# Kernel tuning notes

Hardware: AMD Instinct MI355X
Metric: run time of the kernel (lower is better)

Reference implementation:

```python
import jax, jax.numpy as jnp
import numpy as np

N_NODES = 50000


def graph_conv(h, src, dst, W, b, num_nodes):
    """GCN-style conv: transform node features, then sum messages over edges.
    h: [N, Din], W: [Din, Dout] -> out: [N, Dout].
    """
    m = (h @ W)[src]                                   # [E, Dout] per-edge messages
    agg = jax.ops.segment_sum(m, dst, num_segments=num_nodes)  # [N, Dout]
    return agg + b


def setup_inputs() -> dict:
    key = jax.random.key(0)
    ks = jax.random.split(key, 8)
    N, E, D = N_NODES, 800000, 128
    s = 1.0 / np.sqrt(2 * D)
    return {
        "node_feature": jax.random.normal(ks[0], (N, D), jnp.float32),
        "H_prev": jax.random.normal(ks[1], (N, D), jnp.float32),
        "edge_index": jax.random.randint(ks[2], (2, E), 0, N, jnp.int32),
        "W_main": jax.random.normal(ks[3], (D, D), jnp.float32) / np.sqrt(D),
        "b_main": jnp.zeros((D,), jnp.float32),
        "W_z": jax.random.normal(ks[4], (2 * D, D), jnp.float32) * s,
        "b_z": jnp.zeros((D,), jnp.float32),
        "W_r": jax.random.normal(ks[5], (2 * D, D), jnp.float32) * s,
        "b_r": jnp.zeros((D,), jnp.float32),
        "W_h": jax.random.normal(ks[6], (2 * D, D), jnp.float32) * s,
        "b_h": jnp.zeros((D,), jnp.float32),
    }


def reference(node_feature, H_prev, edge_index, W_main, b_main,
              W_z, b_z, W_r, b_r, W_h, b_h):
    N = node_feature.shape[0]
    src, dst = edge_index[0], edge_index[1]
    # main message-passing layer + post-layer activation (ReLU)
    X = jax.nn.relu(graph_conv(node_feature, src, dst, W_main, b_main, N))
    # GRU-gated graph convolutions
    cat_zr = jnp.concatenate([X, H_prev], axis=1)       # [N, 2D]
    Z = jax.nn.sigmoid(graph_conv(cat_zr, src, dst, W_z, b_z, N))
    R = jax.nn.sigmoid(graph_conv(cat_zr, src, dst, W_r, b_r, N))
    cat_h = jnp.concatenate([X, R * H_prev], axis=1)
    H_tilde = jnp.tanh(graph_conv(cat_h, src, dst, W_h, b_h, N))
    H_out = Z * H_prev + (1.0 - Z) * H_tilde
    return H_out
```

## Files before the change

### kernel.cpp

```cpp
#include <hip/hip_runtime.h>
#include <hip/hip_fp16.h>
#include <math.h>

typedef _Float16 f16;
typedef f16 f16x2 __attribute__((ext_vector_type(2)));
typedef f16 f16x4 __attribute__((ext_vector_type(4)));
typedef f16 f16x8 __attribute__((ext_vector_type(8)));
typedef float f32x4_t __attribute__((ext_vector_type(4)));

__device__ __forceinline__ float sigmoidf(float x) {
  return 1.0f / (1.0f + __expf(-x));
}

#define GLDS16(gp, lp)                                                     \
  __builtin_amdgcn_global_load_lds(                                        \
      (const __attribute__((address_space(1))) void*)(gp),                 \
      (__attribute__((address_space(3))) void*)(lp), 16, 0, 0)

__global__ void zero_ints(int* __restrict__ p, int n) {
  int i = blockIdx.x * blockDim.x + threadIdx.x;
  if (i < n) p[i] = 0;
}

__global__ void count_kernel(const int* __restrict__ dst, int* __restrict__ cnt, int E) {
  int base = (blockIdx.x * blockDim.x + threadIdx.x) * 4;
  if (base + 3 < E) {
    int4 d = *(const int4*)&dst[base];
    atomicAdd(&cnt[d.x], 1);
    atomicAdd(&cnt[d.y], 1);
    atomicAdd(&cnt[d.z], 1);
    atomicAdd(&cnt[d.w], 1);
  } else {
    for (int e = base; e < E; ++e) atomicAdd(&cnt[dst[e]], 1);
  }
}

__global__ __launch_bounds__(1024) void scan_local(const int* __restrict__ cnt,
                                                   int* __restrict__ off,
                                                   int* __restrict__ psum, int n) {
  __shared__ int wsum[16];
  const int tid = threadIdx.x, lane = tid & 63, wid = tid >> 6;
  int i = blockIdx.x * 1024 + tid;
  int v = (i < n) ? cnt[i] : 0;
  int x = v;
  #pragma unroll
  for (int d = 1; d < 64; d <<= 1) { int y = __shfl_up(x, d); if (lane >= d) x += y; }
  if (lane == 63) wsum[wid] = x;
  __syncthreads();
  if (wid == 0) {
    int ws = (lane < 16) ? wsum[lane] : 0;
    #pragma unroll
    for (int d = 1; d < 16; d <<= 1) { int y = __shfl_up(ws, d); if (lane >= d) ws += y; }
    if (lane < 16) wsum[lane] = ws;
  }
  __syncthreads();
  int excl = x - v + (wid ? wsum[wid - 1] : 0);
  if (i < n) off[i] = excl;
  if (tid == 1023) psum[blockIdx.x] = wsum[15];
}

__global__ __launch_bounds__(1024) void scan_carry(int* __restrict__ psum,
                                                   int* __restrict__ off,
                                                   int* __restrict__ cur, int nb, int n) {
  __shared__ int wsum[16];
  const int tid = threadIdx.x, lane = tid & 63, wid = tid >> 6;
  int v = (tid < nb) ? psum[tid] : 0;
  int x = v;
  #pragma unroll
  for (int d = 1; d < 64; d <<= 1) { int y = __shfl_up(x, d); if (lane >= d) x += y; }
  if (lane == 63) wsum[wid] = x;
  __syncthreads();
  if (wid == 0) {
    int ws = (lane < 16) ? wsum[lane] : 0;
    #pragma unroll
    for (int d = 1; d < 16; d <<= 1) { int y = __shfl_up(ws, d); if (lane >= d) ws += y; }
    if (lane < 16) wsum[lane] = ws;
  }
  __syncthreads();
  int excl = x - v + (wid ? wsum[wid - 1] : 0);
  if (tid < nb) psum[tid] = excl;
  if (tid == 1023) { off[n] = wsum[15]; cur[n] = wsum[15]; }
}

__global__ __launch_bounds__(1024) void scan_add(int* __restrict__ off, int* __restrict__ cur,
                                                 const int* __restrict__ psum, int n) {
  int i = blockIdx.x * 1024 + threadIdx.x;
  if (i < n) {
    int t = off[i] + psum[blockIdx.x];
    off[i] = t;
    cur[i] = t;
  }
}

template <typename IDX>
__global__ void fill_kernel(const int* __restrict__ src, const int* __restrict__ dst,
                            int* __restrict__ cur, IDX* __restrict__ eidx, int E) {
  int base = (blockIdx.x * blockDim.x + threadIdx.x) * 4;
  if (base + 3 < E) {
    int4 d = *(const int4*)&dst[base];
    int4 s = *(const int4*)&src[base];
    int p0 = atomicAdd(&cur[d.x], 1);
    int p1 = atomicAdd(&cur[d.y], 1);
    int p2 = atomicAdd(&cur[d.z], 1);
    int p3 = atomicAdd(&cur[d.w], 1);
    eidx[p0] = (IDX)s.x;
    eidx[p1] = (IDX)s.y;
    eidx[p2] = (IDX)s.z;
    eidx[p3] = (IDX)s.w;
  } else {
    for (int e = base; e < E; ++e) {
      int p = atomicAdd(&cur[dst[e]], 1);
      eidx[p] = (IDX)src[e];
    }
  }
}

__global__ void pack_nfh(const float* __restrict__ nf, const float* __restrict__ H,
                         f16* __restrict__ P0, int N) {
  int gid = blockIdx.x * blockDim.x + threadIdx.x;
  int w = gid >> 6;
  if (w >= N) return;
  int lane = threadIdx.x & 63;
  const float* S = (lane < 32) ? nf : H;
  int c = (lane & 31) * 4;
  float4 u = *(const float4*)&S[(size_t)w * 128 + c];
  f16x4 o = {(f16)u.x, (f16)u.y, (f16)u.z, (f16)u.w};
  *(f16x4*)&P0[(size_t)w * 256 + (lane < 32 ? 0 : 128) + c] = o;
}

__global__ void wtrans_all(const float* __restrict__ Wm, const float* __restrict__ Wz,
                           const float* __restrict__ Wr, const float* __restrict__ Wh,
                           f16* __restrict__ WtM, f16* __restrict__ WtZR,
                           f16* __restrict__ WtH) {
  __shared__ float tile[32][33];
  const float* W;
  f16* O;
  int K;
  switch (blockIdx.z) {
    case 0: W = Wm; O = WtM; K = 128; break;
    case 1: W = Wz; O = WtZR; K = 256; break;
    case 2: W = Wr; O = WtZR + 128 * 256; K = 256; break;
    default: W = Wh; O = WtH; K = 256; break;
  }
  int bk = blockIdx.x * 32, bn = blockIdx.y * 32;
  if (bk >= K) return;
  int tx = threadIdx.x, ty = threadIdx.y;
  #pragma unroll
  for (int i = 0; i < 4; ++i)
    tile[ty + 8 * i][tx] = W[(size_t)(bk + ty + 8 * i) * 128 + bn + tx];
  __syncthreads();
  #pragma unroll
  for (int i = 0; i < 4; ++i)
    O[(size_t)(bn + ty + 8 * i) * K + bk + tx] = (f16)tile[tx][ty + 8 * i];
}

template <int COLS, typename IDX>
__global__ __launch_bounds__(256) void gather(const f16* __restrict__ P,
                                              const int* __restrict__ off,
                                              const IDX* __restrict__ eidx,
                                              f16* __restrict__ O, int N) {
  int gid = blockIdx.x * blockDim.x + threadIdx.x;
  int w = __builtin_amdgcn_readfirstlane(gid >> 6);
  if (w >= N) return;
  const int lane = threadIdx.x & 63;
  const int beg = off[w], end = off[w + 1];
  const char* base = (const char*)P;
  constexpr int SH = (COLS == 256) ? 9 : 8;
  int j = beg;
  if constexpr (COLS == 256) {
    const int lb = lane * 8;
    float a0 = 0.f, a1 = 0.f, a2 = 0.f, a3 = 0.f;
    for (; j + 8 <= end; j += 8) {
      f16x4 v[8];
      #pragma unroll
      for (int u = 0; u < 8; ++u)
        v[u] = *(const f16x4*)(base + (((int)eidx[j + u]) << SH) + lb);
      #pragma unroll
      for (int u = 0; u < 8; ++u) {
        a0 += (float)v[u].x; a1 += (float)v[u].y;
        a2 += (float)v[u].z; a3 += (float)v[u].w;
      }
    }
    for (; j < end; ++j) {
      f16x4 v = *(const f16x4*)(base + (((int)eidx[j]) << SH) + lb);
      a0 += (float)v.x; a1 += (float)v.y; a2 += (float)v.z; a3 += (float)v.w;
    }
    f16x4 o = {(f16)a0, (f16)a1, (f16)a2, (f16)a3};
    *(f16x4*)&O[(size_t)w * 256 + lane * 4] = o;
  } else {
    const int lb = lane * 4;
    float a0 = 0.f, a1 = 0.f;
    for (; j + 8 <= end; j += 8) {
      f16x2 v[8];
      #pragma unroll
      for (int u = 0; u < 8; ++u)
        v[u] = *(const f16x2*)(base + (((int)eidx[j + u]) << SH) + lb);
      #pragma unroll
      for (int u = 0; u < 8; ++u) { a0 += (float)v[u].x; a1 += (float)v[u].y; }
    }
    for (; j < end; ++j) {
      f16x2 v = *(const f16x2*)(base + (((int)eidx[j]) << SH) + lb);
      a0 += (float)v.x; a1 += (float)v.y;
    }
    f16x2 o = {(f16)a0, (f16)a1};
    *(f16x2*)&O[(size_t)w * 128 + lane * 2] = o;
  }
}

template <int TERMS, int EPI>
__global__ __launch_bounds__(256) void gemm_mfma(
    const f16* __restrict__ A0, int lda0, const f16* __restrict__ A1, int lda1,
    const f16* __restrict__ Wt,
    const float* __restrict__ b0, const float* __restrict__ b1,
    const float* __restrict__ H, const f16* __restrict__ Zh,
    f16* __restrict__ O0, f16* __restrict__ O1, float* __restrict__ Ofp, int N) {
  constexpr int KTOT = TERMS * 128;
  __shared__ __align__(16) f16 As[64][64];
  __shared__ __align__(16) f16 Bs[128][64];
  f16* Asf = &As[0][0];
  f16* Bsf = &Bs[0][0];
  const int tid = threadIdx.x;
  const int l = tid & 63;
  const int wv = __builtin_amdgcn_readfirstlane(tid >> 6);
  const int fr = l & 15;
  const int q = l >> 4;
  const int brow = blockIdx.x * 64;
  const int coff = blockIdx.y * 128;
  const int rowA = wv * 16 + fr;
  const int sl8 = l >> 3, sg = l & 7;

  f32x4_t acc[8];
  #pragma unroll
  for (int n = 0; n < 8; ++n) acc[n] = (f32x4_t)0.0f;

  #pragma unroll
  for (int kk = 0; kk < KTOT; kk += 64) {
    const bool sel1 = (TERMS == 2) && (kk >= 128);
    const f16* __restrict__ A = sel1 ? A1 : A0;
    const int lda = sel1 ? lda1 : lda0;
    const int klocal = kk & 127;

    __syncthreads();
    #pragma unroll
    for (int c = 0; c < 2; ++c) {
      int chunk = wv + c * 4;
      int row = chunk * 8 + sl8;
      int gs = sg ^ (row & 7);
      int grow = brow + row;
      if (grow > N - 1) grow = N - 1;
      GLDS16(A + (size_t)grow * lda + klocal + gs * 8, Asf + chunk * 512);
    }
    #pragma unroll
    for (int c = 0; c < 4; ++c) {
      int chunk = wv + c * 4;
      int col = chunk * 8 + sl8;
      int gs = sg ^ (col & 7);
      GLDS16(Wt + (size_t)(coff + col) * KTOT + kk + gs * 8, Bsf + chunk * 512);
    }
    asm volatile("s_waitcnt vmcnt(0)" ::: "memory");
    __syncthreads();

    #pragma unroll
    for (int ks = 0; ks < 2; ++ks) {
      f16x8 a = *(const f16x8*)&As[rowA][((ks * 4 + q) ^ (rowA & 7)) * 8];
      f16x8 b[8];
      #pragma unroll
      for (int n = 0; n < 8; ++n) {
        int colB = n * 16 + fr;
        b[n] = *(const f16x8*)&Bs[colB][((ks * 4 + q) ^ (colB & 7)) * 8];
      }
      #pragma unroll
      for (int n = 0; n < 8; ++n)
        acc[n] = __builtin_amdgcn_mfma_f32_16x16x32_f16(a, b[n], acc[n], 0, 0, 0);
    }
  }

  const int row0 = brow + wv * 16 + q * 4;
  #pragma unroll
  for (int n = 0; n < 8; ++n) {
    int colL = n * 16 + fr;
    if (EPI == 0) {
      float bias = b0[colL];
      #pragma unroll
      for (int r = 0; r < 4; ++r) {
        int row = row0 + r;
        if (row < N)
          O0[(size_t)row * 128 + colL] = (f16)fmaxf(acc[n][r] + bias, 0.f);
      }
    } else if (EPI == 1) {
      if (coff == 0) {
        float bias = b0[colL];
        #pragma unroll
        for (int r = 0; r < 4; ++r) {
          int row = row0 + r;
          if (row < N)
            O0[(size_t)row * 128 + colL] = (f16)sigmoidf(acc[n][r] + bias);
        }
      } else {
        float bias = b1[colL];
        #pragma unroll
        for (int r = 0; r < 4; ++r) {
          int row = row0 + r;
          if (row < N) {
            float g = sigmoidf(acc[n][r] + bias) * H[(size_t)row * 128 + colL];
            O1[(size_t)row * 128 + colL] = (f16)g;
          }
        }
      }
    } else {
      float bias = b0[colL];
      #pragma unroll
      for (int r = 0; r < 4; ++r) {
        int row = row0 + r;
        if (row < N) {
          size_t p = (size_t)row * 128 + colL;
          float ht = tanhf(acc[n][r] + bias);
          float z = (float)Zh[p];
          float h = H[p];
          Ofp[p] = z * h + (1.0f - z) * ht;
        }
      }
    }
  }
}


extern "C" void kernel_launch(void* const* d_in, const int* in_sizes, int n_in,
                              void* d_out, int out_size, void* d_ws, size_t ws_size,
                              hipStream_t stream) {
  const float* nf = (const float*)d_in[0];
  const float* H  = (const float*)d_in[1];
  const int*   ei = (const int*)d_in[2];
  const float* Wm = (const float*)d_in[3];
  const float* bm = (const float*)d_in[4];
  const float* Wz = (const float*)d_in[5];
  const float* bz = (const float*)d_in[6];
  const float* Wr = (const float*)d_in[7];
  const float* br = (const float*)d_in[8];
  const float* Wh = (const float*)d_in[9];
  const float* bh = (const float*)d_in[10];
  float* out = (float*)d_out;

  const int N = in_sizes[0] / 128;
  const int E = in_sizes[2] / 2;
  const int* src = ei;
  const int* dst = ei + E;

  char* ws = (char*)d_ws;
  size_t o = 0;
  auto alloc = [&](size_t bytes) {
    char* p = ws + o;
    o = (o + bytes + 511) & ~(size_t)511;
    return p;
  };
  const int nb = (N + 1023) / 1024;
  int* cnt    = (int*)alloc((size_t)N * 4);
  int* off    = (int*)alloc((size_t)(N + 1) * 4);
  int* cur    = (int*)alloc((size_t)(N + 1) * 4);
  void* eidx  = (void*)alloc((size_t)E * 4);
  int* psum   = (int*)alloc((size_t)nb * 4);
  f16* WtM    = (f16*)alloc((size_t)128 * 128 * 2);
  f16* WtZR   = (f16*)alloc((size_t)256 * 256 * 2);
  f16* WtH    = (f16*)alloc((size_t)128 * 256 * 2);
  f16* P0     = (f16*)alloc((size_t)N * 256 * 2);
  f16* X      = (f16*)alloc((size_t)N * 128 * 2);
  f16* AX     = (f16*)alloc((size_t)N * 128 * 2);
  f16* G      = (f16*)alloc((size_t)N * 128 * 2);
  f16* AP0    = (f16*)d_out;
  f16* Zh     = X;
  f16* AG     = P0;

  const bool small = (N <= 65535);

  zero_ints<<<(N + 255) / 256, 256, 0, stream>>>(cnt, N);
  const int qblk = ((E + 3) / 4 + 255) / 256;
  count_kernel<<<qblk, 256, 0, stream>>>(dst, cnt, E);
  scan_local<<<nb, 1024, 0, stream>>>(cnt, off, psum, N);
  scan_carry<<<1, 1024, 0, stream>>>(psum, off, cur, nb, N);
  scan_add<<<nb, 1024, 0, stream>>>(off, cur, psum, N);
  if (small)
    fill_kernel<unsigned short><<<qblk, 256, 0, stream>>>(src, dst, cur, (unsigned short*)eidx, E);
  else
    fill_kernel<int><<<qblk, 256, 0, stream>>>(src, dst, cur, (int*)eidx, E);

  wtrans_all<<<dim3(8, 4, 4), dim3(32, 8), 0, stream>>>(Wm, Wz, Wr, Wh, WtM, WtZR, WtH);
  const int gblk = (N * 64 + 255) / 256;
  pack_nfh<<<gblk, 256, 0, stream>>>(nf, H, P0, N);

  const int mblk = (N + 63) / 64;

  if (small)
    gather<256, unsigned short><<<gblk, 256, 0, stream>>>(P0, off, (const unsigned short*)eidx, AP0, N);
  else
    gather<256, int><<<gblk, 256, 0, stream>>>(P0, off, (const int*)eidx, AP0, N);

  gemm_mfma<1, 0><<<dim3(mblk, 1), 256, 0, stream>>>(
      AP0, 256, nullptr, 0, WtM, bm, nullptr, nullptr, nullptr, X, nullptr, nullptr, N);

  if (small)
    gather<128, unsigned short><<<gblk, 256, 0, stream>>>(X, off, (const unsigned short*)eidx, AX, N);
  else
    gather<128, int><<<gblk, 256, 0, stream>>>(X, off, (const int*)eidx, AX, N);

  gemm_mfma<2, 1><<<dim3(mblk, 2), 256, 0, stream>>>(
      AX, 128, AP0 + 128, 256, WtZR, bz, br, H, nullptr, Zh, G, nullptr, N);

  if (small)
    gather<128, unsigned short><<<gblk, 256, 0, stream>>>(G, off, (const unsigned short*)eidx, AG, N);
  else
    gather<128, int><<<gblk, 256, 0, stream>>>(G, off, (const int*)eidx, AG, N);

  gemm_mfma<2, 2><<<dim3(mblk, 1), 256, 0, stream>>>(
      AX, 128, AG, 128, WtH, bh, nullptr, H, Zh, nullptr, nullptr, out, N);
}
```

Before: 304.0 us.

## Bucket-sort CSR build, multi-node-per-wave gather, double-buffered MFMA GEMM

Replaces the per-node atomic count/scan/fill CSR construction with a two-level bucket sort: a coarse 256-node bucket histogram, a partition into bins, then a per-bucket local sort that writes offsets and 16-bit indices. The aim is less global atomic contention and more coherent writes. The gather kernel now packs 2 or 4 nodes per wave with 16-byte loads per lane, cutting idle lanes on low-degree nodes and using wider memory transactions. The GEMM double-buffers LDS so global loads for the next K-tile overlap the MFMAs on the current one, at the cost of twice the shared memory and extra setup kernels.

```diff
diff --git a/kernel.cpp b/kernel.cpp
--- a/kernel.cpp
+++ b/kernel.cpp
@@ -20,6 +20,115 @@
 __global__ void zero_ints(int* __restrict__ p, int n) {
   int i = blockIdx.x * blockDim.x + threadIdx.x;
   if (i < n) p[i] = 0;
+}
+
+__global__ void bucket_hist(const int* __restrict__ dst, int* __restrict__ bcntP,
+                            int E, int NB) {
+  __shared__ int h[256];
+  for (int i = threadIdx.x; i < NB; i += 256) h[i] = 0;
+  __syncthreads();
+  int base = (blockIdx.x * 256 + threadIdx.x) * 4;
+  if (base + 3 < E) {
+    int4 d = *(const int4*)&dst[base];
+    atomicAdd(&h[d.x >> 8], 1);
+    atomicAdd(&h[d.y >> 8], 1);
+    atomicAdd(&h[d.z >> 8], 1);
+    atomicAdd(&h[d.w >> 8], 1);
+  } else {
+    for (int e = base; e < E; ++e) atomicAdd(&h[dst[e] >> 8], 1);
+  }
+  __syncthreads();
+  for (int i = threadIdx.x; i < NB; i += 256)
+    if (h[i]) atomicAdd(&bcntP[i * 16], h[i]);
+}
+
+__global__ __launch_bounds__(256) void bucket_scan(const int* __restrict__ bcntP,
+                                                   int* __restrict__ bbases,
+                                                   int* __restrict__ gcurP, int NB) {
+  __shared__ int wsum[4];
+  const int tid = threadIdx.x, lane = tid & 63, wid = tid >> 6;
+  int v = (tid < NB) ? bcntP[tid * 16] : 0;
+  int x = v;
+  #pragma unroll
+  for (int d = 1; d < 64; d <<= 1) { int y = __shfl_up(x, d); if (lane >= d) x += y; }
+  if (lane == 63) wsum[wid] = x;
+  __syncthreads();
+  if (wid == 0 && lane < 4) {
+    int ws = wsum[lane];
+    #pragma unroll
+    for (int d = 1; d < 4; d <<= 1) { int y = __shfl_up(ws, d); if (lane >= d) ws += y; }
+    wsum[lane] = ws;
+  }
+  __syncthreads();
+  int excl = x - v + (wid ? wsum[wid - 1] : 0);
+  if (tid < NB) { bbases[tid] = excl; gcurP[tid * 16] = excl; }
+  if (tid == NB - 1) bbases[NB] = excl + v;
+}
+
+__global__ void partition_k(const int* __restrict__ src, const int* __restrict__ dst,
+                            int* __restrict__ gcurP, unsigned int* __restrict__ bin,
+                            int E) {
+  int base = (blockIdx.x * 256 + threadIdx.x) * 4;
+  if (base + 3 < E) {
+    int4 d = *(const int4*)&dst[base];
+    int4 s = *(const int4*)&src[base];
+    int p0 = atomicAdd(&gcurP[(d.x >> 8) * 16], 1);
+    int p1 = atomicAdd(&gcurP[(d.y >> 8) * 16], 1);
+    int p2 = atomicAdd(&gcurP[(d.z >> 8) * 16], 1);
+    int p3 = atomicAdd(&gcurP[(d.w >> 8) * 16], 1);
+    bin[p0] = (unsigned int)s.x | ((unsigned int)(d.x & 255) << 16);
+    bin[p1] = (unsigned int)s.y | ((unsigned int)(d.y & 255) << 16);
+    bin[p2] = (unsigned int)s.z | ((unsigned int)(d.z & 255) << 16);
+    bin[p3] = (unsigned int)s.w | ((unsigned int)(d.w & 255) << 16);
+  } else {
+    for (int e = base; e < E; ++e) {
+      int p = atomicAdd(&gcurP[(dst[e] >> 8) * 16], 1);
+      bin[p] = (unsigned int)src[e] | ((unsigned int)(dst[e] & 255) << 16);
+    }
+  }
+}
+
+__global__ __launch_bounds__(256) void bucket_sort(const unsigned int* __restrict__ bin,
+                                                   const int* __restrict__ bbases,
+                                                   unsigned short* __restrict__ eidx,
+                                                   int* __restrict__ off,
+                                                   int N, int NB) {
+  const int b = blockIdx.x;
+  const int bb = bbases[b], be = bbases[b + 1];
+  const int d0 = b << 8;
+  const int ndst = min(256, N - d0);
+  __shared__ int hist[256];
+  __shared__ int lofs[256];
+  __shared__ int cnt2[256];
+  const int tid = threadIdx.x;
+  hist[tid] = 0;
+  cnt2[tid] = 0;
+  __syncthreads();
+  for (int i = bb + tid; i < be; i += 256)
+    atomicAdd(&hist[(bin[i] >> 16) & 255], 1);
+  __syncthreads();
+  if (tid < 64) {
+    int l = tid;
+    int v0 = hist[4 * l], v1 = hist[4 * l + 1], v2 = hist[4 * l + 2], v3 = hist[4 * l + 3];
+    int s1 = v0 + v1, s2 = s1 + v2, t = s2 + v3;
+    int x = t;
+    #pragma unroll
+    for (int d = 1; d < 64; d <<= 1) { int y = __shfl_up(x, d); if (l >= d) x += y; }
+    int basex = x - t;
+    lofs[4 * l] = basex;
+    lofs[4 * l + 1] = basex + v0;
+    lofs[4 * l + 2] = basex + s1;
+    lofs[4 * l + 3] = basex + s2;
+  }
+  __syncthreads();
+  if (tid < ndst) off[d0 + tid] = bb + lofs[tid];
+  if (b == NB - 1 && tid == 0) off[N] = be;
+  for (int i = bb + tid; i < be; i += 256) {
+    unsigned int rec = bin[i];
+    int ld = (rec >> 16) & 255;
+    int p = bb + lofs[ld] + atomicAdd(&cnt2[ld], 1);
+    eidx[p] = (unsigned short)(rec & 0xFFFF);
+  }
 }
 
 __global__ void count_kernel(const int* __restrict__ dst, int* __restrict__ cnt, int E) {
@@ -92,9 +201,8 @@
   }
 }
 
-template <typename IDX>
 __global__ void fill_kernel(const int* __restrict__ src, const int* __restrict__ dst,
-                            int* __restrict__ cur, IDX* __restrict__ eidx, int E) {
+                            int* __restrict__ cur, int* __restrict__ eidx, int E) {
   int base = (blockIdx.x * blockDim.x + threadIdx.x) * 4;
   if (base + 3 < E) {
     int4 d = *(const int4*)&dst[base];
@@ -103,14 +211,11 @@
     int p1 = atomicAdd(&cur[d.y], 1);
     int p2 = atomicAdd(&cur[d.z], 1);
     int p3 = atomicAdd(&cur[d.w], 1);
-    eidx[p0] = (IDX)s.x;
-    eidx[p1] = (IDX)s.y;
-    eidx[p2] = (IDX)s.z;
-    eidx[p3] = (IDX)s.w;
+    eidx[p0] = s.x; eidx[p1] = s.y; eidx[p2] = s.z; eidx[p3] = s.w;
   } else {
     for (int e = base; e < E; ++e) {
       int p = atomicAdd(&cur[dst[e]], 1);
-      eidx[p] = (IDX)src[e];
+      eidx[p] = src[e];
     }
   }
 }
@@ -159,52 +264,40 @@
                                               const int* __restrict__ off,
                                               const IDX* __restrict__ eidx,
                                               f16* __restrict__ O, int N) {
+  constexpr int NG = (COLS == 256) ? 2 : 4;
+  constexpr int GL = 64 / NG;
+  constexpr int SH = (COLS == 256) ? 9 : 8;
   int gid = blockIdx.x * blockDim.x + threadIdx.x;
-  int w = __builtin_amdgcn_readfirstlane(gid >> 6);
-  if (w >= N) return;
-  const int lane = threadIdx.x & 63;
-  const int beg = off[w], end = off[w + 1];
-  const char* base = (const char*)P;
-  constexpr int SH = (COLS == 256) ? 9 : 8;
+  int wave = gid >> 6;
+  int lane = threadIdx.x & 63;
+  int g = lane / GL, lg = lane % GL;
+  int node = wave * NG + g;
+  if (node >= N) return;
+  const int beg = off[node], end = off[node + 1];
+  const char* base = (const char*)P + lg * 16;
+  float a0 = 0.f, a1 = 0.f, a2 = 0.f, a3 = 0.f;
+  float a4 = 0.f, a5 = 0.f, a6 = 0.f, a7 = 0.f;
   int j = beg;
-  if constexpr (COLS == 256) {
-    const int lb = lane * 8;
-    float a0 = 0.f, a1 = 0.f, a2 = 0.f, a3 = 0.f;
-    for (; j + 8 <= end; j += 8) {
-      f16x4 v[8];
-      #pragma unroll
-      for (int u = 0; u < 8; ++u)
-        v[u] = *(const f16x4*)(base + (((int)eidx[j + u]) << SH) + lb);
-      #pragma unroll
-      for (int u = 0; u < 8; ++u) {
-        a0 += (float)v[u].x; a1 += (float)v[u].y;
-        a2 += (float)v[u].z; a3 += (float)v[u].w;
-      }
-    }
-    for (; j < end; ++j) {
-      f16x4 v = *(const f16x4*)(base + (((int)eidx[j]) << SH) + lb);
-      a0 += (float)v.x; a1 += (float)v.y; a2 += (float)v.z; a3 += (float)v.w;
-    }
-    f16x4 o = {(f16)a0, (f16)a1, (f16)a2, (f16)a3};
-    *(f16x4*)&O[(size_t)w * 256 + lane * 4] = o;
-  } else {
-    const int lb = lane * 4;
-    float a0 = 0.f, a1 = 0.f;
-    for (; j + 8 <= end; j += 8) {
-      f16x2 v[8];
-      #pragma unroll
-      for (int u = 0; u < 8; ++u)
-        v[u] = *(const f16x2*)(base + (((int)eidx[j + u]) << SH) + lb);
-      #pragma unroll
-      for (int u = 0; u < 8; ++u) { a0 += (float)v[u].x; a1 += (float)v[u].y; }
-    }
-    for (; j < end; ++j) {
-      f16x2 v = *(const f16x2*)(base + (((int)eidx[j]) << SH) + lb);
-      a0 += (float)v.x; a1 += (float)v.y;
-    }
-    f16x2 o = {(f16)a0, (f16)a1};
-    *(f16x2*)&O[(size_t)w * 128 + lane * 2] = o;
-  }
+  for (; j + 8 <= end; j += 8) {
+    f16x8 v[8];
+    #pragma unroll
+    for (int u = 0; u < 8; ++u)
+      v[u] = *(const f16x8*)(base + (((int)eidx[j + u]) << SH));
+    #pragma unroll
+    for (int u = 0; u < 8; ++u) {
+      a0 += (float)v[u][0]; a1 += (float)v[u][1];
+      a2 += (float)v[u][2]; a3 += (float)v[u][3];
+      a4 += (float)v[u][4]; a5 += (float)v[u][5];
+      a6 += (float)v[u][6]; a7 += (float)v[u][7];
+    }
+  }
+  for (; j < end; ++j) {
+    f16x8 v = *(const f16x8*)(base + (((int)eidx[j]) << SH));
+    a0 += (float)v[0]; a1 += (float)v[1]; a2 += (float)v[2]; a3 += (float)v[3];
+    a4 += (float)v[4]; a5 += (float)v[5]; a6 += (float)v[6]; a7 += (float)v[7];
+  }
+  f16x8 o = {(f16)a0, (f16)a1, (f16)a2, (f16)a3, (f16)a4, (f16)a5, (f16)a6, (f16)a7};
+  *(f16x8*)&O[(size_t)node * COLS + lg * 8] = o;
 }
 
 template <int TERMS, int EPI>
@@ -215,10 +308,9 @@
     const float* __restrict__ H, const f16* __restrict__ Zh,
     f16* __restrict__ O0, f16* __restrict__ O1, float* __restrict__ Ofp, int N) {
   constexpr int KTOT = TERMS * 128;
-  __shared__ __align__(16) f16 As[64][64];
-  __shared__ __align__(16) f16 Bs[128][64];
-  f16* Asf = &As[0][0];
-  f16* Bsf = &Bs[0][0];
+  constexpr int T = KTOT / 64;
+  __shared__ __align__(16) f16 As[2][64][64];
+  __shared__ __align__(16) f16 Bs[2][128][64];
   const int tid = threadIdx.x;
   const int l = tid & 63;
   const int wv = __builtin_amdgcn_readfirstlane(tid >> 6);
@@ -233,14 +325,14 @@
   #pragma unroll
   for (int n = 0; n < 8; ++n) acc[n] = (f32x4_t)0.0f;
 
-  #pragma unroll
-  for (int kk = 0; kk < KTOT; kk += 64) {
-    const bool sel1 = (TERMS == 2) && (kk >= 128);
+  auto stage = [&](int t, int buf) {
+    const bool sel1 = (TERMS == 2) && (t >= 2);
     const f16* __restrict__ A = sel1 ? A1 : A0;
     const int lda = sel1 ? lda1 : lda0;
-    const int klocal = kk & 127;
-
-    __syncthreads();
+    const int klocal = (t & 1) * 64;
+    const int kk = t * 64;
+    f16* Asf = &As[buf][0][0];
+    f16* Bsf = &Bs[buf][0][0];
     #pragma unroll
     for (int c = 0; c < 2; ++c) {
       int chunk = wv + c * 4;
@@ -257,22 +349,34 @@
       int gs = sg ^ (col & 7);
       GLDS16(Wt + (size_t)(coff + col) * KTOT + kk + gs * 8, Bsf + chunk * 512);
     }
-    asm volatile("s_waitcnt vmcnt(0)" ::: "memory");
-    __syncthreads();
-
+  };
+
+  stage(0, 0);
+  #pragma unroll
+  for (int t = 0; t < T; ++t) {
+    if (t + 1 < T) {
+      stage(t + 1, (t + 1) & 1);
+      asm volatile("s_waitcnt vmcnt(6)" ::: "memory");
+    } else {
+      asm volatile("s_waitcnt vmcnt(0)" ::: "memory");
+    }
+    __builtin_amdgcn_s_barrier();
+    const int buf = t & 1;
     #pragma unroll
     for (int ks = 0; ks < 2; ++ks) {
-      f16x8 a = *(const f16x8*)&As[rowA][((ks * 4 + q) ^ (rowA & 7)) * 8];
-      f16x8 b[8];
+      f16x8 a = *(const f16x8*)&As[buf][rowA][((ks * 4 + q) ^ (rowA & 7)) * 8];
+      f16x8 bfr[8];
       #pragma unroll
       for (int n = 0; n < 8; ++n) {
         int colB = n * 16 + fr;
-        b[n] = *(const f16x8*)&Bs[colB][((ks * 4 + q) ^ (colB & 7)) * 8];
+        bfr[n] = *(const f16x8*)&Bs[buf][colB][((ks * 4 + q) ^ (colB & 7)) * 8];
       }
       #pragma unroll
       for (int n = 0; n < 8; ++n)
-        acc[n] = __builtin_amdgcn_mfma_f32_16x16x32_f16(a, b[n], acc[n], 0, 0, 0);
-    }
+        acc[n] = __builtin_amdgcn_mfma_f32_16x16x32_f16(a, bfr[n], acc[n], 0, 0, 0);
+    }
+    asm volatile("s_waitcnt lgkmcnt(0)" ::: "memory");
+    __builtin_amdgcn_s_barrier();
   }
 
   const int row0 = brow + wv * 16 + q * 4;
@@ -353,12 +457,17 @@
     o = (o + bytes + 511) & ~(size_t)511;
     return p;
   };
-  const int nb = (N + 1023) / 1024;
-  int* cnt    = (int*)alloc((size_t)N * 4);
+  const int NB = (N + 255) >> 8;
+  const int nbch = (N + 1023) / 1024;
+  int* bcntP  = (int*)alloc((size_t)NB * 16 * 4);
+  int* gcurP  = (int*)alloc((size_t)NB * 16 * 4);
+  int* bbases = (int*)alloc((size_t)(NB + 1) * 4);
+  unsigned int* bin = (unsigned int*)alloc((size_t)E * 4);
   int* off    = (int*)alloc((size_t)(N + 1) * 4);
   int* cur    = (int*)alloc((size_t)(N + 1) * 4);
+  int* cnt    = (int*)alloc((size_t)N * 4);
+  int* psum   = (int*)alloc((size_t)nbch * 4);
   void* eidx  = (void*)alloc((size_t)E * 4);
-  int* psum   = (int*)alloc((size_t)nb * 4);
   f16* WtM    = (f16*)alloc((size_t)128 * 128 * 2);
   f16* WtZR   = (f16*)alloc((size_t)256 * 256 * 2);
   f16* WtH    = (f16*)alloc((size_t)128 * 256 * 2);
@@ -370,45 +479,52 @@
   f16* Zh     = X;
   f16* AG     = P0;
 
-  const bool small = (N <= 65535);
-
-  zero_ints<<<(N + 255) / 256, 256, 0, stream>>>(cnt, N);
+  const bool small = (N <= 65536);
   const int qblk = ((E + 3) / 4 + 255) / 256;
-  count_kernel<<<qblk, 256, 0, stream>>>(dst, cnt, E);
-  scan_local<<<nb, 1024, 0, stream>>>(cnt, off, psum, N);
-  scan_carry<<<1, 1024, 0, stream>>>(psum, off, cur, nb, N);
-  scan_add<<<nb, 1024, 0, stream>>>(off, cur, psum, N);
+
+  if (small) {
+    zero_ints<<<(NB * 16 + 255) / 256, 256, 0, stream>>>(bcntP, NB * 16);
+    bucket_hist<<<qblk, 256, 0, stream>>>(dst, bcntP, E, NB);
+    bucket_scan<<<1, 256, 0, stream>>>(bcntP, bbases, gcurP, NB);
+    partition_k<<<qblk, 256, 0, stream>>>(src, dst, gcurP, bin, E);
+    bucket_sort<<<NB, 256, 0, stream>>>(bin, bbases, (unsigned short*)eidx, off, N, NB);
+  } else {
+    zero_ints<<<(N + 255) / 256, 256, 0, stream>>>(cnt, N);
+    count_kernel<<<qblk, 256, 0, stream>>>(dst, cnt, E);
+    scan_local<<<nbch, 1024, 0, stream>>>(cnt, off, psum, N);
+    scan_carry<<<1, 1024, 0, stream>>>(psum, off, cur, nbch, N);
+    scan_add<<<nbch, 1024, 0, stream>>>(off, cur, psum, N);
+    fill_kernel<<<qblk, 256, 0, stream>>>(src, dst, cur, (int*)eidx, E);
+  }
+
+  wtrans_all<<<dim3(8, 4, 4), dim3(32, 8), 0, stream>>>(Wm, Wz, Wr, Wh, WtM, WtZR, WtH);
+  const int pblk = (N * 64 + 255) / 256;
+  pack_nfh<<<pblk, 256, 0, stream>>>(nf, H, P0, N);
+
+  const int mblk = (N + 63) / 64;
+  const int g256 = (N + 7) / 8;
+  const int g128 = (N + 15) / 16;
+
   if (small)
-    fill_kernel<unsigned short><<<qblk, 256, 0, stream>>>(src, dst, cur, (unsigned short*)eidx, E);
+    gather<256, unsigned short><<<g256, 256, 0, stream>>>(P0, off, (const unsigned short*)eidx, AP0, N);
   else
-    fill_kernel<int><<<qblk, 256, 0, stream>>>(src, dst, cur, (int*)eidx, E);
-
-  wtrans_all<<<dim3(8, 4, 4), dim3(32, 8), 0, stream>>>(Wm, Wz, Wr, Wh, WtM, WtZR, WtH);
-  const int gblk = (N * 64 + 255) / 256;
-  pack_nfh<<<gblk, 256, 0, stream>>>(nf, H, P0, N);
-
-  const int mblk = (N + 63) / 64;
-
-  if (small)
-    gather<256, unsigned short><<<gblk, 256, 0, stream>>>(P0, off, (const unsigned short*)eidx, AP0, N);
-  else
-    gather<256, int><<<gblk, 256, 0, stream>>>(P0, off, (const int*)eidx, AP0, N);
+    gather<256, int><<<g256, 256, 0, stream>>>(P0, off, (const int*)eidx, AP0, N);
 
   gemm_mfma<1, 0><<<dim3(mblk, 1), 256, 0, stream>>>(
       AP0, 256, nullptr, 0, WtM, bm, nullptr, nullptr, nullptr, X, nullptr, nullptr, N);
 
   if (small)
-    gather<128, unsigned short><<<gblk, 256, 0, stream>>>(X, off, (const unsigned short*)eidx, AX, N);
+    gather<128, unsigned short><<<g128, 256, 0, stream>>>(X, off, (const unsigned short*)eidx, AX, N);
   else
-    gather<128, int><<<gblk, 256, 0, stream>>>(X, off, (const int*)eidx, AX, N);
+    gather<128, int><<<g128, 256, 0, stream>>>(X, off, (const int*)eidx, AX, N);
 
   gemm_mfma<2, 1><<<dim3(mblk, 2), 256, 0, stream>>>(
       AX, 128, AP0 + 128, 256, WtZR, bz, br, H, nullptr, Zh, G, nullptr, N);
 
   if (small)
-    gather<128, unsigned short><<<gblk, 256, 0, stream>>>(G, off, (const unsigned short*)eidx, AG, N);
+    gather<128, unsigned short><<<g128, 256, 0, stream>>>(G, off, (const unsigned short*)eidx, AG, N);
   else
-    gather<128, int><<<gblk, 256, 0, stream>>>(G, off, (const int*)eidx, AG, N);
+    gather<128, int><<<g128, 256, 0, stream>>>(G, off, (const int*)eidx, AG, N);
 
   gemm_mfma<2, 2><<<dim3(mblk, 1), 256, 0, stream>>>(
       AX, 128, AG, 128, WtH, bh, nullptr, H, Zh, nullptr, nullptr, out, N);
```

Measured after the change: 354.3 us. 1.17x slower.
